# Kernel tuning notes

Hardware: AMD Instinct MI355X
Metric: run time of the kernel (lower is better)

Reference implementation:

```python
import jax, jax.numpy as jnp
import numpy as np

T, WS, SHIFT, HEADS, DIM = 5, (8, 8), (4, 4), 6, 192
HEAD_DIM = DIM // HEADS
SCALE = HEAD_DIM ** -0.5
MLP_HID = 4 * DIM
TABLE_LEN = (T * 2 * WS[0] - 1) * (2 * WS[1] - 1)


def _rel_index():
    # exact replica of WindowAttention.__init__ index construction (t,h,w coords)
    ct, ch, cw = np.arange(T), np.arange(WS[0]), np.arange(WS[1])
    coords = np.stack(np.meshgrid(ct, ch, cw, indexing='ij')).reshape(3, -1)
    rel = (coords[:, :, None] - coords[:, None, :]).transpose(1, 2, 0).astype(np.int64)
    rel[:, :, 0] += WS[0] - 1
    rel[:, :, 1] += WS[1] - 1
    rel[:, :, 0] *= 2 * WS[1] - 1
    return jnp.asarray(rel.sum(-1))  # (N, N)


def _attn_mask(H, W):
    # standard shifted-window mask on (H,W); identical across T, so tile (T,T)
    img = np.zeros((H, W), np.float32)
    cnt = 0
    for hs in (slice(0, -WS[0]), slice(-WS[0], -SHIFT[0]), slice(-SHIFT[0], None)):
        for ws_ in (slice(0, -WS[1]), slice(-WS[1], -SHIFT[1]), slice(-SHIFT[1], None)):
            img[hs, ws_] = cnt
            cnt += 1
    img = img.reshape(H // WS[0], WS[0], W // WS[1], WS[1]).transpose(0, 2, 1, 3)
    img = img.reshape(-1, WS[0] * WS[1])  # (nW, Wh*Ww)
    m = img[:, None, :] - img[:, :, None]
    m = np.where(m != 0, -100.0, 0.0).astype(np.float32)
    return jnp.asarray(np.tile(m, (1, T, T)))  # (nW, T*Wh*Ww, T*Wh*Ww)


def _win_part(x, ws):
    B, t, H, W, C = x.shape
    x = x.reshape(B, t, H // ws[0], ws[0], W // ws[1], ws[1], C)
    return x.transpose(0, 2, 4, 1, 3, 5, 6).reshape(-1, t * ws[0] * ws[1], C)


def _win_rev(w, ws, H, W, t, B):
    x = w.reshape(B, H // ws[0], W // ws[1], t, ws[0], ws[1], -1)
    return x.transpose(0, 3, 1, 4, 2, 5, 6).reshape(B, t, H, W, -1)


def _ln(x, g, b):
    mu = x.mean(-1, keepdims=True)
    var = ((x - mu) ** 2).mean(-1, keepdims=True)
    return (x - mu) * jax.lax.rsqrt(var + 1e-5) * g + b


def _forward(x, ln1_g, ln1_b, qkv_w, qkv_b, rel_bias_table, proj_w, proj_b,
             ln2_g, ln2_b, fc1_w, fc1_b, fc2_w, fc2_b, H, W):
    B, L, C = x.shape
    shortcut = x
    h = _ln(x, ln1_g, ln1_b)
    qkv = h @ qkv_w.T + qkv_b                                   # (B, L, 3C)
    qkv = qkv.reshape(B, T, H, W, 3 * C)
    qkv = jnp.roll(qkv, (-SHIFT[0], -SHIFT[1]), axis=(2, 3))
    qkv = _win_part(qkv, WS)                                    # (B_, N, 3C)
    B_, N, _ = qkv.shape
    qkv = qkv.reshape(B_, N, 3, HEADS, HEAD_DIM).transpose(2, 0, 3, 1, 4)
    q, k, v = qkv[0], qkv[1], qkv[2]
    attn = jnp.einsum('bhnd,bhmd->bhnm', q * SCALE, k)          # (B_, H, N, N)
    bias = rel_bias_table[_rel_index()].transpose(2, 0, 1)      # (heads, N, N)
    attn = attn + bias[None]
    mask = _attn_mask(H, W)                                     # (nW, N, N)
    nW = mask.shape[0]
    attn = attn.reshape(B_ // nW, nW, HEADS, N, N) + mask[None, :, None]
    attn = jax.nn.softmax(attn.reshape(B_, HEADS, N, N), axis=-1)
    out = jnp.einsum('bhnm,bhmd->bhnd', attn, v)
    out = out.transpose(0, 2, 1, 3).reshape(B_, N, C)
    out = out @ proj_w.T + proj_b
    out = _win_rev(out, WS, H, W, T, B)
    out = jnp.roll(out, (SHIFT[0], SHIFT[1]), axis=(2, 3)).reshape(B, L, C)
    x = shortcut + out
    h = _ln(x, ln2_g, ln2_b)
    h = jax.nn.gelu(h @ fc1_w.T + fc1_b, approximate=False) @ fc2_w.T + fc2_b
    return x + h


def setup_inputs() -> dict:
    key = jax.random.key(0)
    ks = jax.random.split(key, 8)
    B, Himg, Wimg = 2, 64, 64
    L = T * Himg * Wimg
    s = 0.02
    return {
        'x': jax.random.normal(ks[0], (B, L, DIM), jnp.float32),
        'ln1_g': jnp.ones((DIM,), jnp.float32),
        'ln1_b': jnp.zeros((DIM,), jnp.float32),
        'qkv_w': jax.random.normal(ks[1], (3 * DIM, DIM), jnp.float32) * s,
        'qkv_b': jnp.zeros((3 * DIM,), jnp.float32),
        'rel_bias_table': jax.random.normal(ks[2], (TABLE_LEN, HEADS), jnp.float32) * s,
        'proj_w': jax.random.normal(ks[3], (DIM, DIM), jnp.float32) * s,
        'proj_b': jnp.zeros((DIM,), jnp.float32),
        'ln2_g': jnp.ones((DIM,), jnp.float32),
        'ln2_b': jnp.zeros((DIM,), jnp.float32),
        'fc1_w': jax.random.normal(ks[4], (MLP_HID, DIM), jnp.float32) * s,
        'fc1_b': jnp.zeros((MLP_HID,), jnp.float32),
        'fc2_w': jax.random.normal(ks[5], (DIM, MLP_HID), jnp.float32) * s,
        'fc2_b': jnp.zeros((DIM,), jnp.float32),
        'H': Himg,
        'W': Wimg,
    }


def reference(x, ln1_g, ln1_b, qkv_w, qkv_b, rel_bias_table, proj_w, proj_b,
              ln2_g, ln2_b, fc1_w, fc1_b, fc2_w, fc2_b, H, W):
    return _forward(x, ln1_g, ln1_b, qkv_w, qkv_b, rel_bias_table, proj_w, proj_b,
                    ln2_g, ln2_b, fc1_w, fc1_b, fc2_w, fc2_b, H, W)
```

## Files before the change

### kernel.cpp

```cpp
#include <hip/hip_runtime.h>
#include <math.h>

typedef unsigned short u16;
typedef unsigned int u32;
typedef short bf16x8 __attribute__((ext_vector_type(8)));
typedef float f32x4 __attribute__((ext_vector_type(4)));
typedef _Float16 f16x4 __attribute__((ext_vector_type(4)));

#define TT 5
#define HEADS 6
#define HD 32
#define DIM 192
#define NWIN 320
#define LTOK (TT*64*64)
#define BATCH 2
#define MROWS (BATCH*LTOK)
#define QSCALE 0.17677669529663687f
#define LOG2E 1.4426950408889634f
#define QSCALE2 (QSCALE * LOG2E)
#define MASK2 (-100.0f * LOG2E)
#define CVT_BLOCKS 1728

__device__ __forceinline__ u16 f2bf(float f) {
    u32 u = __float_as_uint(f);
    u32 r = (u + 0x7FFFu + ((u >> 16) & 1u)) >> 16;
    return (u16)r;
}
__device__ __forceinline__ float bflo(u32 u) { return __uint_as_float(u << 16); }
__device__ __forceinline__ float bfhi(u32 u) { return __uint_as_float(u & 0xFFFF0000u); }
__device__ __forceinline__ u32 pkh(float a, float b) {
    auto h = __builtin_amdgcn_cvt_pkrtz(a, b);
    return __builtin_bit_cast(u32, h);
}
#if __has_builtin(__builtin_amdgcn_exp2f)
__device__ __forceinline__ float ex2(float x) { return __builtin_amdgcn_exp2f(x); }
#else
__device__ __forceinline__ float ex2(float x) {
    float r; asm("v_exp_f32 %0, %1" : "=v"(r) : "v"(x)); return r;
}
#endif
__device__ __forceinline__ float gelu_fast(float x) {
    float u = fmaf(0.044715f * x * x, x, x);
    float t = ex2(2.302208f * u);
    return x - x * __builtin_amdgcn_rcpf(1.0f + t);
}

__global__ __launch_bounds__(256) void prep_kernel(
    const float* __restrict__ x, const float* __restrict__ g,
    const float* __restrict__ b, u16* __restrict__ out,
    const float* __restrict__ wa, const float* __restrict__ wb,
    const float* __restrict__ wc, const float* __restrict__ wd,
    u16* __restrict__ oa, u16* __restrict__ ob,
    u16* __restrict__ oc, u16* __restrict__ od)
{
    if (blockIdx.x < CVT_BLOCKS) {
        int i = blockIdx.x * 256 + threadIdx.x;
        if (i < 110592)       oa[i]          = f2bf(wa[i]);
        else if (i < 147456)  ob[i - 110592] = f2bf(wb[i - 110592]);
        else if (i < 294912)  oc[i - 147456] = f2bf(wc[i - 147456]);
        else                  od[i - 294912] = f2bf(wd[i - 294912]);
        return;
    }
    int tok  = (blockIdx.x - CVT_BLOCKS) * 4 + (threadIdx.x >> 6);
    int lane = threadIdx.x & 63;
    const float* xr = x + (size_t)tok * DIM;
    float v0 = xr[lane], v1 = xr[lane + 64], v2 = xr[lane + 128];
    float s = v0 + v1 + v2;
    #pragma unroll
    for (int off = 32; off; off >>= 1) s += __shfl_xor(s, off, 64);
    float mu = s * (1.0f / 192.0f);
    float d0 = v0 - mu, d1 = v1 - mu, d2 = v2 - mu;
    float vs = d0 * d0 + d1 * d1 + d2 * d2;
    #pragma unroll
    for (int off = 32; off; off >>= 1) vs += __shfl_xor(vs, off, 64);
    float rstd = rsqrtf(vs * (1.0f / 192.0f) + 1e-5f);
    u16* orow = out + (size_t)tok * DIM;
    orow[lane]       = f2bf(d0 * rstd * g[lane]       + b[lane]);
    orow[lane + 64]  = f2bf(d1 * rstd * g[lane + 64]  + b[lane + 64]);
    orow[lane + 128] = f2bf(d2 * rstd * g[lane + 128] + b[lane + 128]);
}

template<int EPI, int BM>
__global__ __launch_bounds__(256) void mfma_gemm(
    const u16* __restrict__ A, const u16* __restrict__ W,
    const float* __restrict__ bias, void* __restrict__ outp,
    const float* __restrict__ xin, int N, int K)
{
    constexpr int WR = BM / 64;
    constexpr int NA = BM / 32;
    __shared__ u16 As[BM * 64];
    __shared__ u16 Bs[64 * 64];
    const int tid  = threadIdx.x;
    const int lane = tid & 63, wv = tid >> 6;
    const int ln16 = lane & 15, quad = lane >> 4;

    const int flat  = blockIdx.y * gridDim.x + blockIdx.x;
    const int cpx   = (gridDim.x * gridDim.y) >> 3;
    const int nf    = (flat & 7) * cpx + (flat >> 3);
    const int bn    = nf % gridDim.x;
    const int bm    = nf / gridDim.x;

    const int srow = lane >> 3;
    const int sxor = (lane & 7) ^ srow;
    const int acol = sxor * 8;

    f32x4 acc[WR][4] = {};

    for (int k0 = 0; k0 < K; k0 += 64) {
        __syncthreads();
        #pragma unroll
        for (int a = 0; a < NA; ++a) {
            const u16* g = A + (size_t)(bm * BM + a * 32 + wv * 8 + srow) * K + k0 + acol;
            __builtin_amdgcn_global_load_lds(
                (const __attribute__((address_space(1))) u32*)g,
                (__attribute__((address_space(3))) u32*)((char*)As + a * 4096 + wv * 1024),
                16, 0, 0);
        }
        #pragma unroll
        for (int bb = 0; bb < 2; ++bb) {
            const u16* g = W + (size_t)(bn * 64 + bb * 32 + wv * 8 + srow) * K + k0 + acol;
            __builtin_amdgcn_global_load_lds(
                (const __attribute__((address_space(1))) u32*)g,
                (__attribute__((address_space(3))) u32*)((char*)Bs + bb * 4096 + wv * 1024),
                16, 0, 0);
        }
        __syncthreads();
        #pragma unroll
        for (int s = 0; s < 2; ++s) {
            bf16x8 af[WR], bf[4];
            #pragma unroll
            for (int i = 0; i < WR; ++i) {
                int r = wv * (16 * WR) + i * 16 + ln16;
                int slot = (s * 4 + quad) ^ (r & 7);
                af[i] = *(const bf16x8*)((const char*)As + r * 128 + slot * 16);
            }
            #pragma unroll
            for (int j = 0; j < 4; ++j) {
                int r = j * 16 + ln16;
                int slot = (s * 4 + quad) ^ (r & 7);
                bf[j] = *(const bf16x8*)((const char*)Bs + r * 128 + slot * 16);
            }
            #pragma unroll
            for (int i = 0; i < WR; ++i)
                #pragma unroll
                for (int j = 0; j < 4; ++j)
                    acc[i][j] = __builtin_amdgcn_mfma_f32_16x16x32_bf16(
                        af[i], bf[j], acc[i][j], 0, 0, 0);
        }
    }

    #pragma unroll
    for (int i = 0; i < WR; ++i) {
        int gr0 = bm * BM + wv * (16 * WR) + i * 16 + quad * 4;
        #pragma unroll
        for (int j = 0; j < 4; ++j) {
            int gc = bn * 64 + j * 16 + ln16;
            float bv = bias[gc];
            #pragma unroll
            for (int rr = 0; rr < 4; ++rr) {
                int gr = gr0 + rr;
                float val = acc[i][j][rr] + bv;
                if (EPI == 0) {
                    ((u16*)outp)[(size_t)gr * N + gc] = f2bf(val);
                } else if (EPI == 1) {
                    ((u16*)outp)[(size_t)gr * N + gc] = f2bf(gelu_fast(val));
                } else {
                    ((float*)outp)[(size_t)gr * N + gc] += val;
                }
            }
        }
    }
}

__global__ __launch_bounds__(256) void proj_ln_kernel(
    const u16* __restrict__ A,
    const u16* __restrict__ W,
    const float* __restrict__ bias,
    const float* __restrict__ xin,
    float* __restrict__ out,
    const float* __restrict__ g2, const float* __restrict__ b2,
    u16* __restrict__ hout)
{
    __shared__ u16 As[64 * 64];
    __shared__ u16 Bs[192 * 64];
    const int tid  = threadIdx.x;
    const int lane = tid & 63, wv = tid >> 6;
    const int ln16 = lane & 15, quad = lane >> 4;
    const int srow = lane >> 3;
    const int acol = ((lane & 7) ^ srow) * 8;

    const int flat = blockIdx.x;
    const int bm   = (flat & 7) * (gridDim.x >> 3) + (flat >> 3);

    f32x4 acc[12] = {};

    for (int k0 = 0; k0 < DIM; k0 += 64) {
        __syncthreads();
        #pragma unroll
        for (int a = 0; a < 2; ++a) {
            const u16* g = A + (size_t)(bm * 64 + a * 32 + wv * 8 + srow) * DIM + k0 + acol;
            __builtin_amdgcn_global_load_lds(
                (const __attribute__((address_space(1))) u32*)g,
                (__attribute__((address_space(3))) u32*)((char*)As + a * 4096 + wv * 1024),
                16, 0, 0);
        }
        #pragma unroll
        for (int bb = 0; bb < 6; ++bb) {
            const u16* g = W + (size_t)(bb * 32 + wv * 8 + srow) * DIM + k0 + acol;
            __builtin_amdgcn_global_load_lds(
                (const __attribute__((address_space(1))) u32*)g,
                (__attribute__((address_space(3))) u32*)((char*)Bs + bb * 4096 + wv * 1024),
                16, 0, 0);
        }
        __syncthreads();
        #pragma unroll
        for (int s = 0; s < 2; ++s) {
            int ra = wv * 16 + ln16;
            int slota = (s * 4 + quad) ^ (ra & 7);
            bf16x8 af = *(const bf16x8*)((const char*)As + ra * 128 + slota * 16);
            #pragma unroll
            for (int nt = 0; nt < 12; ++nt) {
                int r = nt * 16 + ln16;
                int slot = (s * 4 + quad) ^ (r & 7);
                bf16x8 bf = *(const bf16x8*)((const char*)Bs + r * 128 + slot * 16);
                acc[nt] = __builtin_amdgcn_mfma_f32_16x16x32_bf16(af, bf, acc[nt], 0, 0, 0);
            }
        }
    }

    const int gr0 = bm * 64 + wv * 16 + quad * 4;
    float s1[4] = {}, s2[4] = {};
    #pragma unroll
    for (int nt = 0; nt < 12; ++nt) {
        int gc = nt * 16 + ln16;
        float bv = bias[gc];
        #pragma unroll
        for (int rr = 0; rr < 4; ++rr) {
            size_t dst = (size_t)(gr0 + rr) * DIM + gc;
            float ov = xin[dst] + acc[nt][rr] + bv;
            out[dst] = ov;
            s1[rr] += ov;
            s2[rr] += ov * ov;
        }
    }
    #pragma unroll
    for (int rr = 0; rr < 4; ++rr) {
        #pragma unroll
        for (int off = 8; off; off >>= 1) {
            s1[rr] += __shfl_xor(s1[rr], off, 64);
            s2[rr] += __shfl_xor(s2[rr], off, 64);
        }
    }
    float mu[4], rstd[4];
    #pragma unroll
    for (int rr = 0; rr < 4; ++rr) {
        mu[rr] = s1[rr] * (1.0f / 192.0f);
        float var = s2[rr] * (1.0f / 192.0f) - mu[rr] * mu[rr];
        rstd[rr] = rsqrtf(var + 1e-5f);
    }
    #pragma unroll
    for (int nt = 0; nt < 12; ++nt) {
        int gc = nt * 16 + ln16;
        float bv = bias[gc];
        float gg = g2[gc], bb = b2[gc];
        #pragma unroll
        for (int rr = 0; rr < 4; ++rr) {
            size_t dst = (size_t)(gr0 + rr) * DIM + gc;
            float ov = xin[dst] + acc[nt][rr] + bv;
            hout[dst] = f2bf((ov - mu[rr]) * rstd[rr] * gg + bb);
        }
    }
}

__global__ __launch_bounds__(640) void attn_kernel(
    const u16* __restrict__ qkv, const float* __restrict__ table,
    u16* __restrict__ attout)
{
    const int head = blockIdx.x % HEADS;
    const int b_   = blockIdx.x / HEADS;
    const int b = b_ >> 6, hb = (b_ >> 3) & 7, wb = b_ & 7;
    const int tid = threadIdx.x;
    const int lane = tid & 63, wv = tid >> 6;
    const int ln16 = lane & 15, quad = lane >> 4;

    __shared__ u16 Ks[320 * 40];
    __shared__ u16 Vt[32 * 328];
    __shared__ u16 meta[320];
    __shared__ float tbl[188];

    if (tid < 320) {
        int n = tid;
        int t1 = n >> 6, r1 = (n >> 3) & 7, c1 = n & 7;
        int h1 = hb * 8 + r1, w1 = wb * 8 + c1;
        int l1 = t1 * 4096 + ((h1 + 4) & 63) * 64 + ((w1 + 4) & 63);
        const u16* src = qkv + ((size_t)b * LTOK + l1) * (3 * DIM) + head * HD;
        const uint4* k4 = (const uint4*)(src + DIM);
        #pragma unroll
        for (int i = 0; i < 4; ++i)
            *(uint4*)(Ks + n * 40 + i * 8) = k4[i];
        const uint4* v4 = (const uint4*)(src + 2 * DIM);
        #pragma unroll
        for (int i = 0; i < 4; ++i) {
            uint4 u = v4[i];
            u32 ws[4] = {u.x, u.y, u.z, u.w};
            #pragma unroll
            for (int j = 0; j < 4; ++j) {
                u32 hb2 = pkh(bflo(ws[j]), bfhi(ws[j]));
                int d = i * 8 + j * 2;
                Vt[d * 328 + n]       = (u16)(hb2 & 0xFFFF);
                Vt[(d + 1) * 328 + n] = (u16)(hb2 >> 16);
            }
        }
        int off = (7 - t1) * 15 + 7 - r1 - c1;
        int rh = h1 < 56 ? 0 : (h1 < 60 ? 1 : 2);
        int rw = w1 < 56 ? 0 : (w1 < 60 ? 1 : 2);
        meta[n] = (u16)(off | ((rh * 3 + rw) << 8));
        if (n < 187) tbl[n] = table[n * HEADS + head] * LOG2E;
    }

    bf16x8 qf[2];
    int basen[2], myreg[2];
    #pragma unroll
    for (int qt = 0; qt < 2; ++qt) {
        int nq = wv * 32 + qt * 16 + ln16;
        int t1 = nq >> 6, r1 = (nq >> 3) & 7, c1 = nq & 7;
        int h1 = hb * 8 + r1, w1 = wb * 8 + c1;
        int l1 = t1 * 4096 + ((h1 + 4) & 63) * 64 + ((w1 + 4) & 63);
        qf[qt] = *(const bf16x8*)(qkv + ((size_t)b * LTOK + l1) * (3 * DIM)
                                  + head * HD + quad * 8);
        basen[qt] = t1 * 15 + r1 + c1;
        int rh = h1 < 56 ? 0 : (h1 < 60 ? 1 : 2);
        int rw = w1 < 56 ? 0 : (w1 < 60 ? 1 : 2);
        myreg[qt] = rh * 3 + rw;
    }

    __syncthreads();

    f32x4 o[2][2] = {};
    float l_[2] = {};
    const f32x4 zero = {};

    #pragma unroll 1
    for (int c = 0; c < 10; ++c) {
        int kb = c * 32;
        bf16x8 af0 = *(const bf16x8*)(Ks + (kb + ln16) * 40 + quad * 8);
        bf16x8 af1 = *(const bf16x8*)(Ks + (kb + 16 + ln16) * 40 + quad * 8);
        f16x4 va[2][2];
        #pragma unroll
        for (int dt = 0; dt < 2; ++dt)
            #pragma unroll
            for (int kt = 0; kt < 2; ++kt)
                va[dt][kt] = *(const f16x4*)(Vt + (dt * 16 + ln16) * 328
                                             + kb + kt * 16 + quad * 4);
        ushort4 m4a = *(const ushort4*)(meta + kb + quad * 4);
        ushort4 m4b = *(const ushort4*)(meta + kb + 16 + quad * 4);
        u16 mta[4] = {m4a.x, m4a.y, m4a.z, m4a.w};
        u16 mtb[4] = {m4b.x, m4b.y, m4b.z, m4b.w};

        #pragma unroll
        for (int qt = 0; qt < 2; ++qt) {
            f32x4 s0 = __builtin_amdgcn_mfma_f32_16x16x32_bf16(af0, qf[qt], zero, 0, 0, 0);
            f32x4 s1 = __builtin_amdgcn_mfma_f32_16x16x32_bf16(af1, qf[qt], zero, 0, 0, 0);
            float p[8];
            #pragma unroll
            for (int r = 0; r < 4; ++r) {
                int ma = mta[r], mb = mtb[r];
                float va0 = fmaf(s0[r], QSCALE2, tbl[basen[qt] + (ma & 0xFF)]);
                float vb0 = fmaf(s1[r], QSCALE2, tbl[basen[qt] + (mb & 0xFF)]);
                p[r]     = va0 + (((ma >> 8) == myreg[qt]) ? 0.0f : MASK2);
                p[4 + r] = vb0 + (((mb >> 8) == myreg[qt]) ? 0.0f : MASK2);
            }
            float ls = 0.0f;
            #pragma unroll
            for (int j = 0; j < 8; ++j) { p[j] = ex2(p[j]); ls += p[j]; }
            l_[qt] += ls;
            uint2 pk0 = { pkh(p[0], p[1]), pkh(p[2], p[3]) };
            uint2 pk1 = { pkh(p[4], p[5]), pkh(p[6], p[7]) };
            f16x4 pf0 = __builtin_bit_cast(f16x4, pk0);
            f16x4 pf1 = __builtin_bit_cast(f16x4, pk1);
            #pragma unroll
            for (int dt = 0; dt < 2; ++dt) {
                o[qt][dt] = __builtin_amdgcn_mfma_f32_16x16x16f16(va[dt][0], pf0, o[qt][dt], 0, 0, 0);
                o[qt][dt] = __builtin_amdgcn_mfma_f32_16x16x16f16(va[dt][1], pf1, o[qt][dt], 0, 0, 0);
            }
        }
    }

    #pragma unroll
    for (int qt = 0; qt < 2; ++qt) {
        float lt = l_[qt];
        lt += __shfl_xor(lt, 16, 64);
        lt += __shfl_xor(lt, 32, 64);
        float inv = 1.0f / lt;
        int nq = wv * 32 + qt * 16 + ln16;
        u16* dst = attout + ((size_t)(b_ * NWIN + nq)) * DIM + head * HD + quad * 4;
        #pragma unroll
        for (int dt = 0; dt < 2; ++dt) {
            u32 w0 = (u32)f2bf(o[qt][dt][0] * inv) | ((u32)f2bf(o[qt][dt][1] * inv) << 16);
            u32 w1 = (u32)f2bf(o[qt][dt][2] * inv) | ((u32)f2bf(o[qt][dt][3] * inv) << 16);
            uint2 st = {w0, w1};
            *(uint2*)(dst + dt * 16) = st;
        }
    }
}

extern "C" void kernel_launch(void* const* d_in, const int* in_sizes, int n_in,
                              void* d_out, int out_size, void* d_ws, size_t ws_size,
                              hipStream_t stream)
{
    (void)in_sizes; (void)n_in; (void)out_size; (void)ws_size;
    const float* x      = (const float*)d_in[0];
    const float* ln1_g  = (const float*)d_in[1];
    const float* ln1_b  = (const float*)d_in[2];
    const float* qkv_w  = (const float*)d_in[3];
    const float* qkv_b  = (const float*)d_in[4];
    const float* table  = (const float*)d_in[5];
    const float* proj_w = (const float*)d_in[6];
    const float* proj_b = (const float*)d_in[7];
    const float* ln2_g  = (const float*)d_in[8];
    const float* ln2_b  = (const float*)d_in[9];
    const float* fc1_w  = (const float*)d_in[10];
    const float* fc1_b  = (const float*)d_in[11];
    const float* fc2_w  = (const float*)d_in[12];
    const float* fc2_b  = (const float*)d_in[13];
    float* out = (float*)d_out;

    u16* wsu     = (u16*)d_ws;
    u16* h_buf   = wsu;
    u16* qkv_buf = wsu + (size_t)MROWS * DIM;
    u16* att_buf = wsu + (size_t)MROWS * (4 * DIM);
    u16* fc1_buf = wsu + (size_t)MROWS * DIM;
    u16* wq = wsu + (size_t)MROWS * (5 * DIM);
    u16* wp = wq + 3 * DIM * DIM;
    u16* w1 = wp + DIM * DIM;
    u16* w2 = w1 + 4 * DIM * DIM;

    prep_kernel<<<CVT_BLOCKS + MROWS / 4, 256, 0, stream>>>(
        x, ln1_g, ln1_b, h_buf,
        qkv_w, proj_w, fc1_w, fc2_w, wq, wp, w1, w2);

    mfma_gemm<0, 128><<<dim3(3 * DIM / 64, MROWS / 128), 256, 0, stream>>>(
        h_buf, wq, qkv_b, qkv_buf, nullptr, 3 * DIM, DIM);
    attn_kernel<<<128 * HEADS, 640, 0, stream>>>(qkv_buf, table, att_buf);
    proj_ln_kernel<<<MROWS / 64, 256, 0, stream>>>(
        att_buf, wp, proj_b, x, out, ln2_g, ln2_b, h_buf);
    mfma_gemm<1, 128><<<dim3(4 * DIM / 64, MROWS / 128), 256, 0, stream>>>(
        h_buf, w1, fc1_b, fc1_buf, nullptr, 4 * DIM, DIM);
    mfma_gemm<3, 64><<<dim3(DIM / 64, MROWS / 64), 256, 0, stream>>>(
        fc1_buf, w2, fc2_b, out, nullptr, DIM, 4 * DIM);
}
```

Before: 244.4 us.

## Halve proj_ln row tile and split columns across wave pairs

The proj+residual+LayerNorm kernel now processes 32 rows per block instead of 64, doubling the grid. Each pair of waves shares a 16-row tile and splits the 192 output columns in half, which halves per-wave accumulators. Row statistics are combined across the two waves through a small shared array with an added barrier. The aim is more blocks and lower register pressure for better occupancy, at the cost of loading the full weight tile twice as often per row.

```diff
diff --git a/kernel.cpp b/kernel.cpp
--- a/kernel.cpp
+++ b/kernel.cpp
@@ -181,27 +181,29 @@
     const float* __restrict__ g2, const float* __restrict__ b2,
     u16* __restrict__ hout)
 {
-    __shared__ u16 As[64 * 64];
+    __shared__ u16 As[32 * 64];
     __shared__ u16 Bs[192 * 64];
+    __shared__ float sx[4][16][2];
     const int tid  = threadIdx.x;
     const int lane = tid & 63, wv = tid >> 6;
     const int ln16 = lane & 15, quad = lane >> 4;
     const int srow = lane >> 3;
     const int acol = ((lane & 7) ^ srow) * 8;
+    const int rtile = wv >> 1;
+    const int chalf = wv & 1;
 
     const int flat = blockIdx.x;
     const int bm   = (flat & 7) * (gridDim.x >> 3) + (flat >> 3);
 
-    f32x4 acc[12] = {};
+    f32x4 acc[6] = {};
 
     for (int k0 = 0; k0 < DIM; k0 += 64) {
         __syncthreads();
-        #pragma unroll
-        for (int a = 0; a < 2; ++a) {
-            const u16* g = A + (size_t)(bm * 64 + a * 32 + wv * 8 + srow) * DIM + k0 + acol;
+        {
+            const u16* g = A + (size_t)(bm * 32 + wv * 8 + srow) * DIM + k0 + acol;
             __builtin_amdgcn_global_load_lds(
                 (const __attribute__((address_space(1))) u32*)g,
-                (__attribute__((address_space(3))) u32*)((char*)As + a * 4096 + wv * 1024),
+                (__attribute__((address_space(3))) u32*)((char*)As + wv * 1024),
                 16, 0, 0);
         }
         #pragma unroll
@@ -215,12 +217,12 @@
         __syncthreads();
         #pragma unroll
         for (int s = 0; s < 2; ++s) {
-            int ra = wv * 16 + ln16;
+            int ra = rtile * 16 + ln16;
             int slota = (s * 4 + quad) ^ (ra & 7);
             bf16x8 af = *(const bf16x8*)((const char*)As + ra * 128 + slota * 16);
             #pragma unroll
-            for (int nt = 0; nt < 12; ++nt) {
-                int r = nt * 16 + ln16;
+            for (int nt = 0; nt < 6; ++nt) {
+                int r = (chalf * 6 + nt) * 16 + ln16;
                 int slot = (s * 4 + quad) ^ (r & 7);
                 bf16x8 bf = *(const bf16x8*)((const char*)Bs + r * 128 + slot * 16);
                 acc[nt] = __builtin_amdgcn_mfma_f32_16x16x32_bf16(af, bf, acc[nt], 0, 0, 0);
@@ -228,11 +230,11 @@
         }
     }
 
-    const int gr0 = bm * 64 + wv * 16 + quad * 4;
+    const int gr0 = bm * 32 + rtile * 16 + quad * 4;
     float s1[4] = {}, s2[4] = {};
     #pragma unroll
-    for (int nt = 0; nt < 12; ++nt) {
-        int gc = nt * 16 + ln16;
+    for (int nt = 0; nt < 6; ++nt) {
+        int gc = (chalf * 6 + nt) * 16 + ln16;
         float bv = bias[gc];
         #pragma unroll
         for (int rr = 0; rr < 4; ++rr) {
@@ -251,16 +253,26 @@
             s2[rr] += __shfl_xor(s2[rr], off, 64);
         }
     }
+    if (ln16 == 0) {
+        #pragma unroll
+        for (int rr = 0; rr < 4; ++rr) {
+            sx[wv][quad * 4 + rr][0] = s1[rr];
+            sx[wv][quad * 4 + rr][1] = s2[rr];
+        }
+    }
+    __syncthreads();
     float mu[4], rstd[4];
     #pragma unroll
     for (int rr = 0; rr < 4; ++rr) {
-        mu[rr] = s1[rr] * (1.0f / 192.0f);
-        float var = s2[rr] * (1.0f / 192.0f) - mu[rr] * mu[rr];
+        float t1 = s1[rr] + sx[wv ^ 1][quad * 4 + rr][0];
+        float t2 = s2[rr] + sx[wv ^ 1][quad * 4 + rr][1];
+        mu[rr] = t1 * (1.0f / 192.0f);
+        float var = t2 * (1.0f / 192.0f) - mu[rr] * mu[rr];
         rstd[rr] = rsqrtf(var + 1e-5f);
     }
     #pragma unroll
-    for (int nt = 0; nt < 12; ++nt) {
-        int gc = nt * 16 + ln16;
+    for (int nt = 0; nt < 6; ++nt) {
+        int gc = (chalf * 6 + nt) * 16 + ln16;
         float bv = bias[gc];
         float gg = g2[gc], bb = b2[gc];
         #pragma unroll
@@ -442,7 +454,7 @@
     mfma_gemm<0, 128><<<dim3(3 * DIM / 64, MROWS / 128), 256, 0, stream>>>(
         h_buf, wq, qkv_b, qkv_buf, nullptr, 3 * DIM, DIM);
     attn_kernel<<<128 * HEADS, 640, 0, stream>>>(qkv_buf, table, att_buf);
-    proj_ln_kernel<<<MROWS / 64, 256, 0, stream>>>(
+    proj_ln_kernel<<<MROWS / 32, 256, 0, stream>>>(
         att_buf, wp, proj_b, x, out, ln2_g, ln2_b, h_buf);
     mfma_gemm<1, 128><<<dim3(4 * DIM / 64, MROWS / 128), 256, 0, stream>>>(
         h_buf, w1, fc1_b, fc1_buf, nullptr, 4 * DIM, DIM);
```

Measured after the change: 244.6 us. No clear change (+0.1%).
